# Kernel optimization log

Hardware: AMD Instinct MI355X
Metric: run time of the kernel (lower is better)

## Reference

```python
import jax, jax.numpy as jnp
import numpy as np

# module hyper-params (from NLSearch __init__ defaults)
K = 7        # top-k neighbors
PS = 7       # patch size
WS = 8       # search window (ws x ws candidates)
NHEADS = 1
STRIDE0 = 4  # query grid stride
STRIDE1 = 1  # candidate stride within window


def _reflect(i, n):
    # reflect (mirror) out-of-range indices into [0, n)
    i = jnp.where(i < 0, -i, i)
    return jnp.where(i >= n, 2 * (n - 1) - i, i)


def setup_inputs() -> dict:
    key = jax.random.key(0)
    k0, k1 = jax.random.split(key)
    vid0 = jax.random.normal(k0, (1, 3, 32, 256, 256), dtype=jnp.float32)
    vid1 = jax.random.normal(k1, (1, 3, 32, 256, 256), dtype=jnp.float32)
    return {"vid0": vid0, "vid1": vid1}


def _nl_search(vid0, vid1):
    B, T, C, H, W = vid0.shape
    HD = NHEADS
    c = C // HD
    v0 = vid0.reshape(B, T, HD, c, H, W)
    v1 = vid1.reshape(B, T, HD, c, H, W)
    nH = (H - 1) // STRIDE0 + 1
    nW = (W - 1) // STRIDE0 + 1
    qh = jnp.arange(nH) * STRIDE0  # query centers
    qw = jnp.arange(nW) * STRIDE0
    poff = jnp.arange(PS) - PS // 2  # centered patch offsets

    def patches(v, hc, wc):
        # gather reflect-bounded ps x ps patches centered at (hc, wc)
        hi = _reflect(hc[:, None] + poff[None, :], H)  # [nH, PS]
        wi = _reflect(wc[:, None] + poff[None, :], W)  # [nW, PS]
        p = v[:, :, :, :, hi]          # [B,T,HD,c,nH,PS,W]
        p = p[:, :, :, :, :, :, wi]    # [B,T,HD,c,nH,PS,nW,PS]
        return p

    p0 = patches(v0, qh, qw)  # query patches, reused across all shifts
    woff = (jnp.arange(WS) - WS // 2) * STRIDE1
    shifts = jnp.stack(jnp.meshgrid(woff, woff, indexing='ij'), -1).reshape(-1, 2)  # [WS*WS,2]

    def body(carry, s):
        def step(s_):
            p1 = patches(v1, qh + s_[0], qw + s_[1])
            # patch inner product ('prod' search distance)
            return jnp.einsum('bthcnivj,bthcnivj->bthnv', p0, p1)
        return carry, jax.checkpoint(step)(s)

    _, dists = jax.lax.scan(body, 0, shifts)   # [L,B,T,HD,nH,nW]
    dists = jnp.moveaxis(dists, 0, -1)         # [B,T,HD,nH,nW,L]

    # anchor_self: force the self (zero-shift) candidate to rank first,
    # but return its true distance (bump only used for ordering)
    self_idx = (WS // 2) * WS + (WS // 2)
    adj = dists.at[..., self_idx].add(jnp.asarray(1e30, dists.dtype))
    _, top_idx = jax.lax.top_k(adj, K)                       # [B,T,HD,nH,nW,K]
    top_d = jnp.take_along_axis(dists, top_idx, axis=-1)     # [B,T,HD,nH,nW,K]

    # decode flat shift index -> absolute (t,h,w) neighbor coordinates
    dh = (top_idx // WS - WS // 2) * STRIDE1
    dw = (top_idx % WS - WS // 2) * STRIDE1
    hh = _reflect(qh[None, None, None, :, None, None] + dh, H)
    ww = _reflect(qw[None, None, None, None, :, None] + dw, W)
    tt = jnp.broadcast_to(jnp.arange(T)[None, :, None, None, None, None], hh.shape)
    inds = jnp.stack([tt, hh, ww], -1)  # [B,T,HD,nH,nW,K,3]

    Q = T * nH * nW
    dists_out = jnp.transpose(top_d, (0, 2, 1, 3, 4, 5)).reshape(B, HD, Q, K)
    inds_out = jnp.transpose(inds, (0, 2, 1, 3, 4, 5, 6)).reshape(B, HD, Q, K, 3)
    return dists_out, inds_out


def reference(vid0, vid1):
    return _nl_search(vid0, vid1)
```

## Files before the change

### kernel.cpp

```cpp
#include <hip/hip_runtime.h>

#define TT 3
#define CCH 32
#define HH 256
#define WW 256
#define KK 7
#define NQ 64
#define QPB 16
#define V1W 76
#define V1R 14
#define V1N (V1R*V1W)
#define V1P 1080
#define CHC 8
#define NCHUNK 4

__device__ __forceinline__ int refl(int i, int n) {
    i = i < 0 ? -i : i;
    return i >= n ? 2*(n-1) - i : i;
}

__device__ __forceinline__ void gload_lds(const float* g, float* l) {
    __builtin_amdgcn_global_load_lds(
        (const __attribute__((address_space(1))) unsigned int*)g,
        (__attribute__((address_space(3))) unsigned int*)l, 4, 0, 0);
}

__global__ __launch_bounds__(256, 3)
void nls_kernel(const float* __restrict__ vid0, const float* __restrict__ vid1,
                float* __restrict__ out) {
    __shared__ float v1s[CHC * V1P];

    const int bx  = blockIdx.x;
    const int t   = bx >> 8;
    const int rem = bx & 255;
    const int qy  = rem >> 2;
    const int q0  = (rem & 3) * QPB;
    const int qh  = qy * 4;
    const int w0  = 4*q0 - 7;

    const int tid   = threadIdx.x;
    const int qwi   = tid & 15;
    const int c01   = (tid >> 4) & 3;
    const int c2    = (tid >> 6) & 1;
    const int shh   = tid >> 7;
    const int clane = c01 + 4*c2;
    const int qx    = q0 + qwi;

    int off1[5];
#pragma unroll
    for (int k = 0; k < 5; ++k) {
        int idx = tid + 256*k;
        if (idx < V1N) {
            int r = idx / V1W, wi = idx - r*V1W;
            off1[k] = refl(qh + r - 7, HH) * WW + refl(w0 + wi, WW);
        } else off1[k] = 0;
    }

    float acc[4][8];
#pragma unroll
    for (int a = 0; a < 4; ++a)
#pragma unroll
        for (int b = 0; b < 8; ++b) acc[a][b] = 0.f;

    const float* g0t = vid0 + (size_t)t * (CCH*HH*WW);
    const float* g1t = vid1 + (size_t)t * (CCH*HH*WW);

#pragma unroll 1
    for (int s = 0; s < NCHUNK; ++s) {
        __syncthreads();
#pragma unroll
        for (int ch = 0; ch < CHC; ++ch) {
            const float* p1 = g1t + (size_t)(CHC*s + ch) * (HH*WW);
            float* lb = &v1s[ch*V1P + (tid & ~63)];
#pragma unroll
            for (int k = 0; k < 4; ++k)
                gload_lds(p1 + off1[k], lb + 256*k);
            if (tid < V1N - 1024)
                gload_lds(p1 + off1[4], &v1s[ch*V1P + 1024 + (tid & ~63)]);
        }

        const float* p0 = g0t + (size_t)(CHC*s + clane) * (HH*WW);
        float x[7][8];
#pragma unroll
        for (int i = 0; i < 7; ++i) {
            const float* rowp = p0 + refl(qh + i - 3, HH) * WW;
            float4 B = *(const float4*)(rowp + 4*qx);
            float4 A;
            if (qx > 0) A = *(const float4*)(rowp + 4*qx - 4);
            else        A = make_float4(0.f, B.w, B.z, B.y);
            x[i][0]=A.y; x[i][1]=A.z; x[i][2]=A.w;
            x[i][3]=B.x; x[i][4]=B.y; x[i][5]=B.z; x[i][6]=B.w;
        }
        __syncthreads();

        const float* yb = &v1s[clane*V1P + 4*qwi];
#pragma unroll
        for (int rr = 0; rr < 10; ++rr) {
            const float* yp = yb + (4*shh + rr) * V1W;
            float4 Ya = ((const float4*)yp)[0];
            float4 Yb = ((const float4*)yp)[1];
            float4 Yc = ((const float4*)yp)[2];
            float4 Yd = ((const float4*)yp)[3];
            float y[16];
            y[0]=Ya.x;  y[1]=Ya.y;  y[2]=Ya.z;  y[3]=Ya.w;
            y[4]=Yb.x;  y[5]=Yb.y;  y[6]=Yb.z;  y[7]=Yb.w;
            y[8]=Yc.x;  y[9]=Yc.y;  y[10]=Yc.z; y[11]=Yc.w;
            y[12]=Yd.x; y[13]=Yd.y; y[14]=Yd.z; y[15]=Yd.w;
#pragma unroll
            for (int a = 0; a < 4; ++a) {
                const int pi = rr - a;
                if (pi >= 0 && pi < 7) {
#pragma unroll
                    for (int sw = 0; sw < 8; ++sw)
#pragma unroll
                        for (int j = 0; j < 7; ++j)
                            acc[a][sw] += x[pi][j] * y[sw + j];
                }
            }
        }
    }

#pragma unroll
    for (int m = 16; m <= 32; m <<= 1)
#pragma unroll
        for (int a = 0; a < 4; ++a)
#pragma unroll
            for (int b = 0; b < 8; ++b)
                acc[a][b] += __shfl_xor(acc[a][b], m, 64);

    __syncthreads();
    float* dlds = v1s;
    if (c01 == 0) {
#pragma unroll
        for (int a = 0; a < 4; ++a) {
            float* dp = &dlds[c2*1024 + qwi*64 + (shh*4 + a)*8];
            *(float4*)(dp)     = make_float4(acc[a][0], acc[a][1], acc[a][2], acc[a][3]);
            *(float4*)(dp + 4) = make_float4(acc[a][4], acc[a][5], acc[a][6], acc[a][7]);
        }
    }
    __syncthreads();

    {
        const int q16 = tid >> 4;
        const int l16 = tid & 15;
        const float* d0 = &dlds[q16 * 64];
        const float* d1 = d0 + 1024;
        const int j0 = l16 * 4;
        float cv[4];
#pragma unroll
        for (int jj = 0; jj < 4; ++jj) {
            float v = d0[j0 + jj] + d1[j0 + jj];
            if (j0 + jj == 36) v += 1e30f;
            cv[jj] = v;
        }
        unsigned mask = 0;
        const int qxx = q0 + q16;
        const int q   = (t*NQ + qy)*NQ + qxx;
        float* od = out + q*KK;
        float* oi = out + (size_t)TT*NQ*NQ*KK + (size_t)q*KK*3;
        for (int k = 0; k < KK; ++k) {
            float best = -3.4e38f; int bi = 1 << 30;
#pragma unroll
            for (int jj = 0; jj < 4; ++jj)
                if (!(mask & (1u << jj)) && cv[jj] > best) { best = cv[jj]; bi = j0 + jj; }
#pragma unroll
            for (int m = 1; m <= 8; m <<= 1) {
                float ob = __shfl_xor(best, m, 64);
                int  obi = __shfl_xor(bi,  m, 64);
                if (ob > best || (ob == best && obi < bi)) { best = ob; bi = obi; }
            }
            if ((bi >> 2) == l16) mask |= 1u << (bi & 3);
            if (l16 == 0) {
                od[k] = d0[bi] + d1[bi];
                int dh = (bi >> 3) - 4;
                int dw = (bi & 7) - 4;
                oi[k*3 + 0] = (float)t;
                oi[k*3 + 1] = (float)refl(qh + dh, HH);
                oi[k*3 + 2] = (float)refl(qxx*4 + dw, WW);
            }
        }
    }
}

extern "C" void kernel_launch(void* const* d_in, const int* in_sizes, int n_in,
                              void* d_out, int out_size, void* d_ws, size_t ws_size,
                              hipStream_t stream) {
    (void)in_sizes; (void)n_in; (void)d_ws; (void)ws_size; (void)out_size;
    const float* vid0 = (const float*)d_in[0];
    const float* vid1 = (const float*)d_in[1];
    float* out = (float*)d_out;
    nls_kernel<<<dim3(TT * NQ * (NQ / QPB)), dim3(256), 0, stream>>>(vid0, vid1, out);
}
```

Baseline: 124.4 us.

## Stage query patches in LDS and software-pipeline row loads with FMAs

Result: no change. 126.1 us (+1.3%).

```diff
diff --git a/kernel.cpp b/kernel.cpp
--- a/kernel.cpp
+++ b/kernel.cpp
@@ -10,7 +10,10 @@
 #define V1W 76
 #define V1R 14
 #define V1N (V1R*V1W)
-#define V1P 1080
+#define V1P 1088
+#define V0W 72
+#define V0N (7*V0W)
+#define V0P 512
 #define CHC 8
 #define NCHUNK 4
 
@@ -25,10 +28,26 @@
         (__attribute__((address_space(3))) unsigned int*)l, 4, 0, 0);
 }
 
-__global__ __launch_bounds__(256, 3)
+#define XL(I, XA, XB) { const float4* xp = (const float4*)(xbase + (I)*V0W); \
+                        XA = xp[0]; XB = xp[1]; }
+#define YPREF(RR, N0,N1,N2,N3) { \
+    const float4* yp = (const float4*)(ybase + (4*shh + (RR)) * V1W); \
+    N0 = yp[0]; N1 = yp[1]; N2 = yp[2]; N3 = yp[3]; }
+#define YMAT(C0,C1,C2,C3) const float y[16] = { \
+    C0.x,C0.y,C0.z,C0.w, C1.x,C1.y,C1.z,C1.w, \
+    C2.x,C2.y,C2.z,C2.w, C3.x,C3.y,C3.z,C3.w };
+#define FMAROW(AIDX, XA, XB) { \
+    _Pragma("unroll") for (int sw = 0; sw < 8; ++sw) { \
+        acc[AIDX][sw] += XA.x*y[sw+0]; acc[AIDX][sw] += XA.y*y[sw+1]; \
+        acc[AIDX][sw] += XA.z*y[sw+2]; acc[AIDX][sw] += XA.w*y[sw+3]; \
+        acc[AIDX][sw] += XB.x*y[sw+4]; acc[AIDX][sw] += XB.y*y[sw+5]; \
+        acc[AIDX][sw] += XB.z*y[sw+6]; } }
+
+__global__ __launch_bounds__(256)
 void nls_kernel(const float* __restrict__ vid0, const float* __restrict__ vid1,
                 float* __restrict__ out) {
     __shared__ float v1s[CHC * V1P];
+    __shared__ float v0s[CHC * V0P];
 
     const int bx  = blockIdx.x;
     const int t   = bx >> 8;
@@ -44,7 +63,6 @@
     const int c2    = (tid >> 6) & 1;
     const int shh   = tid >> 7;
     const int clane = c01 + 4*c2;
-    const int qx    = q0 + qwi;
 
     int off1[5];
 #pragma unroll
@@ -55,6 +73,15 @@
             off1[k] = refl(qh + r - 7, HH) * WW + refl(w0 + wi, WW);
         } else off1[k] = 0;
     }
+    int off0[2];
+#pragma unroll
+    for (int k = 0; k < 2; ++k) {
+        int idx = tid + 256*k;
+        if (idx < V0N) {
+            int r = idx / V0W, wi = idx - r*V0W;
+            off0[k] = refl(qh + r - 3, HH) * WW + refl(w0 + wi, WW);
+        } else off0[k] = 0;
+    }
 
     float acc[4][8];
 #pragma unroll
@@ -78,46 +105,42 @@
             if (tid < V1N - 1024)
                 gload_lds(p1 + off1[4], &v1s[ch*V1P + 1024 + (tid & ~63)]);
         }
-
-        const float* p0 = g0t + (size_t)(CHC*s + clane) * (HH*WW);
-        float x[7][8];
-#pragma unroll
-        for (int i = 0; i < 7; ++i) {
-            const float* rowp = p0 + refl(qh + i - 3, HH) * WW;
-            float4 B = *(const float4*)(rowp + 4*qx);
-            float4 A;
-            if (qx > 0) A = *(const float4*)(rowp + 4*qx - 4);
-            else        A = make_float4(0.f, B.w, B.z, B.y);
-            x[i][0]=A.y; x[i][1]=A.z; x[i][2]=A.w;
-            x[i][3]=B.x; x[i][4]=B.y; x[i][5]=B.z; x[i][6]=B.w;
+#pragma unroll
+        for (int ch = 0; ch < CHC; ++ch) {
+            const float* p0 = g0t + (size_t)(CHC*s + ch) * (HH*WW);
+            float* lb0 = &v0s[ch*V0P + (tid & ~63)];
+            gload_lds(p0 + off0[0], lb0);
+            if (tid < V0N - 256)
+                gload_lds(p0 + off0[1], lb0 + 256);
         }
         __syncthreads();
 
-        const float* yb = &v1s[clane*V1P + 4*qwi];
-#pragma unroll
-        for (int rr = 0; rr < 10; ++rr) {
-            const float* yp = yb + (4*shh + rr) * V1W;
-            float4 Ya = ((const float4*)yp)[0];
-            float4 Yb = ((const float4*)yp)[1];
-            float4 Yc = ((const float4*)yp)[2];
-            float4 Yd = ((const float4*)yp)[3];
-            float y[16];
-            y[0]=Ya.x;  y[1]=Ya.y;  y[2]=Ya.z;  y[3]=Ya.w;
-            y[4]=Yb.x;  y[5]=Yb.y;  y[6]=Yb.z;  y[7]=Yb.w;
-            y[8]=Yc.x;  y[9]=Yc.y;  y[10]=Yc.z; y[11]=Yc.w;
-            y[12]=Yd.x; y[13]=Yd.y; y[14]=Yd.z; y[15]=Yd.w;
-#pragma unroll
-            for (int a = 0; a < 4; ++a) {
-                const int pi = rr - a;
-                if (pi >= 0 && pi < 7) {
-#pragma unroll
-                    for (int sw = 0; sw < 8; ++sw)
-#pragma unroll
-                        for (int j = 0; j < 7; ++j)
-                            acc[a][sw] += x[pi][j] * y[sw + j];
-                }
-            }
-        }
+        const float* xbase = &v0s[clane*V0P + 4*qwi + 4];
+        const float* ybase = &v1s[clane*V1P + 4*qwi];
+        float4 X0a,X0b,X1a,X1b,X2a,X2b,X3a,X3b,X4a,X4b,X5a,X5b,X6a,X6b;
+        float4 Ya0,Ya1,Ya2,Ya3, Yb0,Yb1,Yb2,Yb3;
+        XL(0, X0a,X0b)
+        YPREF(0, Ya0,Ya1,Ya2,Ya3)
+        { YPREF(1, Yb0,Yb1,Yb2,Yb3) XL(1, X1a,X1b) YMAT(Ya0,Ya1,Ya2,Ya3)
+          FMAROW(0, X0a,X0b) }
+        { YPREF(2, Ya0,Ya1,Ya2,Ya3) XL(2, X2a,X2b) YMAT(Yb0,Yb1,Yb2,Yb3)
+          FMAROW(0, X1a,X1b) FMAROW(1, X0a,X0b) }
+        { YPREF(3, Yb0,Yb1,Yb2,Yb3) XL(3, X3a,X3b) YMAT(Ya0,Ya1,Ya2,Ya3)
+          FMAROW(0, X2a,X2b) FMAROW(1, X1a,X1b) FMAROW(2, X0a,X0b) }
+        { YPREF(4, Ya0,Ya1,Ya2,Ya3) XL(4, X4a,X4b) YMAT(Yb0,Yb1,Yb2,Yb3)
+          FMAROW(0, X3a,X3b) FMAROW(1, X2a,X2b) FMAROW(2, X1a,X1b) FMAROW(3, X0a,X0b) }
+        { YPREF(5, Yb0,Yb1,Yb2,Yb3) XL(5, X5a,X5b) YMAT(Ya0,Ya1,Ya2,Ya3)
+          FMAROW(0, X4a,X4b) FMAROW(1, X3a,X3b) FMAROW(2, X2a,X2b) FMAROW(3, X1a,X1b) }
+        { YPREF(6, Ya0,Ya1,Ya2,Ya3) XL(6, X6a,X6b) YMAT(Yb0,Yb1,Yb2,Yb3)
+          FMAROW(0, X5a,X5b) FMAROW(1, X4a,X4b) FMAROW(2, X3a,X3b) FMAROW(3, X2a,X2b) }
+        { YPREF(7, Yb0,Yb1,Yb2,Yb3) YMAT(Ya0,Ya1,Ya2,Ya3)
+          FMAROW(0, X6a,X6b) FMAROW(1, X5a,X5b) FMAROW(2, X4a,X4b) FMAROW(3, X3a,X3b) }
+        { YPREF(8, Ya0,Ya1,Ya2,Ya3) YMAT(Yb0,Yb1,Yb2,Yb3)
+          FMAROW(1, X6a,X6b) FMAROW(2, X5a,X5b) FMAROW(3, X4a,X4b) }
+        { YPREF(9, Yb0,Yb1,Yb2,Yb3) YMAT(Ya0,Ya1,Ya2,Ya3)
+          FMAROW(2, X6a,X6b) FMAROW(3, X5a,X5b) }
+        { YMAT(Yb0,Yb1,Yb2,Yb3)
+          FMAROW(3, X6a,X6b) }
     }
 
 #pragma unroll
```
